# Optimization experiments

Hardware: AMD Instinct MI355X
Metric: run time of the kernel (lower is better)

Reference implementation:

```python
import jax, jax.numpy as jnp
import numpy as np

N_NODES = 50000
N_EDGES = 800000
IN_CH = 64
HEADS = 8
OUT_CH = 8
LEAKY_ALPHA = 0.3  # Keras LeakyReLU default


def setup_inputs() -> dict:
    key = jax.random.key(0)
    k1, k2, k3, k4, k5 = jax.random.split(key, 5)
    h = jax.random.normal(k1, (N_NODES, IN_CH), dtype=jnp.float32)
    W = jax.random.normal(k2, (2 * IN_CH, HEADS * OUT_CH), dtype=jnp.float32) * 0.1
    a = jax.random.normal(k3, (1, HEADS * OUT_CH), dtype=jnp.float32) * 0.1
    src = jax.random.randint(k4, (N_EDGES,), 0, N_NODES, dtype=jnp.int32)
    tgt = jax.random.randint(k5, (N_EDGES,), 0, N_NODES, dtype=jnp.int32)
    return {"h": h, "W": W, "a": a, "src": src, "tgt": tgt}


def reference(h, W, a, src, tgt):
    # h: [N, C]; W: [2C, H*D]; a: [1, H*D]; src/tgt: [E]
    N = h.shape[0]
    hi = h[src]                                   # [E, C] gather source feats
    hj = h[tgt]                                   # [E, C] gather target feats
    hij = jnp.concatenate([hi, hj], axis=-1)      # [E, 2C]
    e = jax.nn.leaky_relu(hij @ W, negative_slope=LEAKY_ALPHA)  # [E, H*D]
    # (dropout omitted: eval mode)
    e = e * a                                     # broadcast attention vector
    e = e.reshape(-1, HEADS, OUT_CH).sum(axis=-1)  # [E, H] per-head logits
    # segment softmax over target nodes (numerically stable)
    m = jax.ops.segment_max(e, tgt, num_segments=N)   # [N, H]
    ex = jnp.exp(e - m[tgt])                          # [E, H]
    s = jax.ops.segment_sum(ex, tgt, num_segments=N)  # [N, H]
    att = ex / s[tgt]                                 # [E, H]
    # weight source features per head (in_channel == head*out_channel branch)
    msg = hi.reshape(-1, HEADS, OUT_CH) * att[:, :, None]  # [E, H, D]
    out = jax.ops.segment_sum(msg.reshape(-1, HEADS * OUT_CH), tgt, num_segments=N)
    return out  # [N, H*D]
```

## Files before the change

kernel.cpp:

```cpp
#include <hip/hip_runtime.h>
#include <hip/hip_fp16.h>
#include <math.h>

#define ALPHA 0.3f
#define MAXDEG 64
#define LOG2E 1.44269504088896f
#define UVOFF (64 * 68 + 4)

__device__ __forceinline__ unsigned int pack2(float u, float hv) {
    __half2 p = __floats2half2_rn(u, hv);
    unsigned int w;
    __builtin_memcpy(&w, &p, 4);
    return w;
}

__device__ __forceinline__ float2 unpack2(unsigned int w) {
    __half2 p;
    __builtin_memcpy(&p, &w, 4);
    return __half22float2(p);
}

__device__ __forceinline__ float dpp_sum8(float z) {
    int t;
    t = __builtin_amdgcn_mov_dpp(__float_as_int(z), 0xB1, 0xF, 0xF, true);
    z += __int_as_float(t);
    t = __builtin_amdgcn_mov_dpp(__float_as_int(z), 0x4E, 0xF, 0xF, true);
    z += __int_as_float(t);
    t = __builtin_amdgcn_mov_dpp(__float_as_int(z), 0x141, 0xF, 0xF, true);
    z += __int_as_float(t);
    return z;
}

__global__ __launch_bounds__(256) void k_prep(const float* __restrict__ h,
                                              const float* __restrict__ W,
                                              const int* __restrict__ src,
                                              const int* __restrict__ tgt,
                                              unsigned int* __restrict__ g,
                                              float* __restrict__ vbuf,
                                              int* __restrict__ cursor,
                                              unsigned short* __restrict__ srcs,
                                              int N, int E, int nUV) {
    __shared__ float Ws[128 * 68 + 4];
    __shared__ float hs[64 * 68];

    if ((int)blockIdx.x >= nUV) {
        const int q = (blockIdx.x - nUV) * 256 + threadIdx.x;
        const int e = q * 4;
        if (e + 4 <= E) {
            const int4 s4 = *(const int4*)(src + e);
            const int4 t4 = *(const int4*)(tgt + e);
            int p;
            p = atomicAdd(&cursor[t4.x], 1); if (p < MAXDEG) srcs[(size_t)t4.x * MAXDEG + p] = (unsigned short)s4.x;
            p = atomicAdd(&cursor[t4.y], 1); if (p < MAXDEG) srcs[(size_t)t4.y * MAXDEG + p] = (unsigned short)s4.y;
            p = atomicAdd(&cursor[t4.z], 1); if (p < MAXDEG) srcs[(size_t)t4.z * MAXDEG + p] = (unsigned short)s4.z;
            p = atomicAdd(&cursor[t4.w], 1); if (p < MAXDEG) srcs[(size_t)t4.w * MAXDEG + p] = (unsigned short)s4.w;
        } else {
            for (int i = e; i < E; ++i) {
                const int ti = tgt[i];
                const int p = atomicAdd(&cursor[ti], 1);
                if (p < MAXDEG) srcs[(size_t)ti * MAXDEG + p] = (unsigned short)src[i];
            }
        }
        return;
    }

    const int t  = threadIdx.x;
    const int nb = blockIdx.x * 64;

    for (int i = t; i < 128 * 64; i += 256) {
        const int row = i >> 6, col = i & 63;
        const int idx = (row < 64) ? (row * 68 + col) : (UVOFF + (row - 64) * 68 + col);
        Ws[idx] = W[i];
    }
    for (int i = t; i < 64 * 64; i += 256) {
        const int nn = i >> 6, c = i & 63;
        const int n = nb + nn;
        hs[nn * 68 + c] = (n < N) ? h[(size_t)n * 64 + c] : 0.0f;
    }
    __syncthreads();

    const int kk = t & 15;
    const int gn = t >> 4;
    const int colbase = (kk * 8) & 63;
    const int wbase   = (kk < 8) ? 0 : UVOFF;

    float acc[4][8];
#pragma unroll
    for (int i = 0; i < 4; ++i)
#pragma unroll
        for (int j = 0; j < 8; ++j) acc[i][j] = 0.0f;

    for (int c4 = 0; c4 < 64; c4 += 4) {
        float hh4[4][4];
#pragma unroll
        for (int i = 0; i < 4; ++i) {
            const float4 tv = *(const float4*)&hs[(gn * 4 + i) * 68 + c4];
            hh4[i][0] = tv.x; hh4[i][1] = tv.y; hh4[i][2] = tv.z; hh4[i][3] = tv.w;
        }
#pragma unroll
        for (int cc = 0; cc < 4; ++cc) {
            const float* wrow = &Ws[wbase + (c4 + cc) * 68 + colbase];
            const float4 w0 = *(const float4*)(wrow);
            const float4 w1 = *(const float4*)(wrow + 4);
            const float wv[8] = {w0.x, w0.y, w0.z, w0.w, w1.x, w1.y, w1.z, w1.w};
#pragma unroll
            for (int i = 0; i < 4; ++i)
#pragma unroll
                for (int j = 0; j < 8; ++j) acc[i][j] += hh4[i][cc] * wv[j];
        }
    }

#pragma unroll
    for (int i = 0; i < 4; ++i) {
        const int n = nb + gn * 4 + i;
        if (n >= N) continue;
        if (kk < 8) {
            unsigned int w[8];
#pragma unroll
            for (int j = 0; j < 8; ++j)
                w[j] = pack2(acc[i][j], hs[(gn * 4 + i) * 68 + colbase + j]);
            uint4 w0 = {w[0], w[1], w[2], w[3]};
            uint4 w1 = {w[4], w[5], w[6], w[7]};
            *(uint4*)&g[(size_t)n * 64 + colbase]     = w0;
            *(uint4*)&g[(size_t)n * 64 + colbase + 4] = w1;
        } else {
            float4 o0 = {acc[i][0], acc[i][1], acc[i][2], acc[i][3]};
            float4 o1 = {acc[i][4], acc[i][5], acc[i][6], acc[i][7]};
            *(float4*)&vbuf[(size_t)n * 64 + colbase]     = o0;
            *(float4*)&vbuf[(size_t)n * 64 + colbase + 4] = o1;
        }
    }
}

__global__ __launch_bounds__(256) void k_node(const unsigned int* __restrict__ g,
                                              const float* __restrict__ vbuf,
                                              const float* __restrict__ a,
                                              const int* __restrict__ cnt,
                                              const unsigned short* __restrict__ srcs,
                                              float* __restrict__ out, int N) {
    const int wid  = (blockIdx.x * 256 + threadIdx.x) >> 6;
    const int lane = threadIdx.x & 63;
    if (wid >= N) return;

    const float v_l = vbuf[(size_t)wid * 64 + lane];
    const float a_l = a[lane] * LOG2E;
    const int num = min(cnt[wid], MAXDEG);
    const int beg = wid * MAXDEG;

    float l_run = 0.0f, acc = 0.0f;

    int k = 0;
    for (; k + 8 <= num; k += 8) {
        const ushort4 sa = *(const ushort4*)(srcs + beg + k);
        const ushort4 sb = *(const ushort4*)(srcs + beg + k + 4);
        unsigned int w[8];
        w[0] = g[(size_t)sa.x * 64 + lane];
        w[1] = g[(size_t)sa.y * 64 + lane];
        w[2] = g[(size_t)sa.z * 64 + lane];
        w[3] = g[(size_t)sa.w * 64 + lane];
        w[4] = g[(size_t)sb.x * 64 + lane];
        w[5] = g[(size_t)sb.y * 64 + lane];
        w[6] = g[(size_t)sb.z * 64 + lane];
        w[7] = g[(size_t)sb.w * 64 + lane];
#pragma unroll
        for (int j = 0; j < 8; ++j) {
            const float2 f = unpack2(w[j]);
            const float q = f.x + v_l;
            float z = fmaxf(q, q * ALPHA) * a_l;
            z = dpp_sum8(z);
            const float p = __builtin_amdgcn_exp2f(z);
            l_run += p;
            acc = fmaf(f.y, p, acc);
        }
    }
    for (; k < num; ++k) {
        const int s = srcs[beg + k];
        const float2 f = unpack2(g[(size_t)s * 64 + lane]);
        const float q = f.x + v_l;
        float z = fmaxf(q, q * ALPHA) * a_l;
        z = dpp_sum8(z);
        const float p = __builtin_amdgcn_exp2f(z);
        l_run += p;
        acc = fmaf(f.y, p, acc);
    }

    out[(size_t)wid * 64 + lane] = (num > 0) ? (acc / l_run) : 0.0f;
}

extern "C" void kernel_launch(void* const* d_in, const int* in_sizes, int n_in,
                              void* d_out, int out_size, void* d_ws, size_t ws_size,
                              hipStream_t stream) {
    const float* h   = (const float*)d_in[0];
    const float* W   = (const float*)d_in[1];
    const float* a   = (const float*)d_in[2];
    const int*   src = (const int*)d_in[3];
    const int*   tgt = (const int*)d_in[4];
    float* out = (float*)d_out;

    const int N = in_sizes[0] / 64;
    const int E = in_sizes[3];

    unsigned int*   g      = (unsigned int*)d_ws;
    float*          vbuf   = (float*)(g + (size_t)N * 64);
    int*            cursor = (int*)(vbuf + (size_t)N * 64);
    unsigned short* srcs   = (unsigned short*)(cursor + N);

    hipMemsetAsync(cursor, 0, (size_t)N * sizeof(int), stream);

    const int nUV   = (N + 63) / 64;
    const int nFILL = (E / 4 + 255) / 256;
    k_prep<<<nUV + nFILL, 256, 0, stream>>>(h, W, src, tgt, g, vbuf, cursor, srcs, N, E, nUV);
    k_node<<<((size_t)N * 64 + 255) / 256, 256, 0, stream>>>(g, vbuf, a, cursor, srcs, out, N);
}
```

Baseline: 108.0 us.

## Split prep kernel, fold cursor zeroing into UV kernel, read h directly

Replaces the memset plus combined prep kernel with three launches: a UV projection kernel that also zeroes the cursor array, a separate fill kernel, and the node kernel. The UV kernel drops the shared-memory staging of h and reads h rows straight from global memory, which shrinks LDS use and may raise occupancy. This removes the memset call but adds a kernel launch, and the fill phase can no longer overlap with the projection blocks. The cursor zeroing is correct only because each block zeroes 256 entries while (N+63)/64 blocks cover N.

```diff
diff --git a/kernel.cpp b/kernel.cpp
--- a/kernel.cpp
+++ b/kernel.cpp
@@ -31,59 +31,36 @@
     return z;
 }
 
-__global__ __launch_bounds__(256) void k_prep(const float* __restrict__ h,
-                                              const float* __restrict__ W,
-                                              const int* __restrict__ src,
-                                              const int* __restrict__ tgt,
-                                              unsigned int* __restrict__ g,
-                                              float* __restrict__ vbuf,
-                                              int* __restrict__ cursor,
-                                              unsigned short* __restrict__ srcs,
-                                              int N, int E, int nUV) {
-    __shared__ float Ws[128 * 68 + 4];
-    __shared__ float hs[64 * 68];
-
-    if ((int)blockIdx.x >= nUV) {
-        const int q = (blockIdx.x - nUV) * 256 + threadIdx.x;
-        const int e = q * 4;
-        if (e + 4 <= E) {
-            const int4 s4 = *(const int4*)(src + e);
-            const int4 t4 = *(const int4*)(tgt + e);
-            int p;
-            p = atomicAdd(&cursor[t4.x], 1); if (p < MAXDEG) srcs[(size_t)t4.x * MAXDEG + p] = (unsigned short)s4.x;
-            p = atomicAdd(&cursor[t4.y], 1); if (p < MAXDEG) srcs[(size_t)t4.y * MAXDEG + p] = (unsigned short)s4.y;
-            p = atomicAdd(&cursor[t4.z], 1); if (p < MAXDEG) srcs[(size_t)t4.z * MAXDEG + p] = (unsigned short)s4.z;
-            p = atomicAdd(&cursor[t4.w], 1); if (p < MAXDEG) srcs[(size_t)t4.w * MAXDEG + p] = (unsigned short)s4.w;
-        } else {
-            for (int i = e; i < E; ++i) {
-                const int ti = tgt[i];
-                const int p = atomicAdd(&cursor[ti], 1);
-                if (p < MAXDEG) srcs[(size_t)ti * MAXDEG + p] = (unsigned short)src[i];
-            }
-        }
-        return;
-    }
-
-    const int t  = threadIdx.x;
-    const int nb = blockIdx.x * 64;
+__global__ __launch_bounds__(256) void k_uv(const float* __restrict__ h,
+                                            const float* __restrict__ W,
+                                            unsigned int* __restrict__ g,
+                                            float* __restrict__ vbuf,
+                                            int* __restrict__ cursor, int N) {
+    __shared__ float Ws[UVOFF + 64 * 68];
+    const int t = threadIdx.x;
+    const int gidx = blockIdx.x * 256 + t;
+    if (gidx < N) cursor[gidx] = 0;
 
     for (int i = t; i < 128 * 64; i += 256) {
         const int row = i >> 6, col = i & 63;
         const int idx = (row < 64) ? (row * 68 + col) : (UVOFF + (row - 64) * 68 + col);
         Ws[idx] = W[i];
     }
-    for (int i = t; i < 64 * 64; i += 256) {
-        const int nn = i >> 6, c = i & 63;
-        const int n = nb + nn;
-        hs[nn * 68 + c] = (n < N) ? h[(size_t)n * 64 + c] : 0.0f;
-    }
     __syncthreads();
 
+    const int nb = blockIdx.x * 64;
     const int kk = t & 15;
     const int gn = t >> 4;
     const int colbase = (kk * 8) & 63;
     const int wbase   = (kk < 8) ? 0 : UVOFF;
 
+    int nidx[4];
+#pragma unroll
+    for (int i = 0; i < 4; ++i) {
+        int n = nb + gn * 4 + i;
+        nidx[i] = (n < N) ? n : (N - 1);
+    }
+
     float acc[4][8];
 #pragma unroll
     for (int i = 0; i < 4; ++i)
@@ -91,11 +68,11 @@
         for (int j = 0; j < 8; ++j) acc[i][j] = 0.0f;
 
     for (int c4 = 0; c4 < 64; c4 += 4) {
-        float hh4[4][4];
+        float hh[4][4];
 #pragma unroll
         for (int i = 0; i < 4; ++i) {
-            const float4 tv = *(const float4*)&hs[(gn * 4 + i) * 68 + c4];
-            hh4[i][0] = tv.x; hh4[i][1] = tv.y; hh4[i][2] = tv.z; hh4[i][3] = tv.w;
+            const float4 tv = *(const float4*)&h[(size_t)nidx[i] * 64 + c4];
+            hh[i][0] = tv.x; hh[i][1] = tv.y; hh[i][2] = tv.z; hh[i][3] = tv.w;
         }
 #pragma unroll
         for (int cc = 0; cc < 4; ++cc) {
@@ -106,7 +83,7 @@
 #pragma unroll
             for (int i = 0; i < 4; ++i)
 #pragma unroll
-                for (int j = 0; j < 8; ++j) acc[i][j] += hh4[i][cc] * wv[j];
+                for (int j = 0; j < 8; ++j) acc[i][j] += hh[i][cc] * wv[j];
         }
     }
 
@@ -115,10 +92,12 @@
         const int n = nb + gn * 4 + i;
         if (n >= N) continue;
         if (kk < 8) {
+            const float4 h0 = *(const float4*)&h[(size_t)n * 64 + colbase];
+            const float4 h1 = *(const float4*)&h[(size_t)n * 64 + colbase + 4];
+            const float hv[8] = {h0.x, h0.y, h0.z, h0.w, h1.x, h1.y, h1.z, h1.w};
             unsigned int w[8];
 #pragma unroll
-            for (int j = 0; j < 8; ++j)
-                w[j] = pack2(acc[i][j], hs[(gn * 4 + i) * 68 + colbase + j]);
+            for (int j = 0; j < 8; ++j) w[j] = pack2(acc[i][j], hv[j]);
             uint4 w0 = {w[0], w[1], w[2], w[3]};
             uint4 w1 = {w[4], w[5], w[6], w[7]};
             *(uint4*)&g[(size_t)n * 64 + colbase]     = w0;
@@ -128,6 +107,29 @@
             float4 o1 = {acc[i][4], acc[i][5], acc[i][6], acc[i][7]};
             *(float4*)&vbuf[(size_t)n * 64 + colbase]     = o0;
             *(float4*)&vbuf[(size_t)n * 64 + colbase + 4] = o1;
+        }
+    }
+}
+
+__global__ __launch_bounds__(256) void k_fill(const int* __restrict__ src,
+                                              const int* __restrict__ tgt,
+                                              int* __restrict__ cursor,
+                                              unsigned short* __restrict__ srcs, int E) {
+    const int q = blockIdx.x * 256 + threadIdx.x;
+    const int e = q * 4;
+    if (e + 4 <= E) {
+        const int4 s4 = *(const int4*)(src + e);
+        const int4 t4 = *(const int4*)(tgt + e);
+        int p;
+        p = atomicAdd(&cursor[t4.x], 1); if (p < MAXDEG) srcs[(size_t)t4.x * MAXDEG + p] = (unsigned short)s4.x;
+        p = atomicAdd(&cursor[t4.y], 1); if (p < MAXDEG) srcs[(size_t)t4.y * MAXDEG + p] = (unsigned short)s4.y;
+        p = atomicAdd(&cursor[t4.z], 1); if (p < MAXDEG) srcs[(size_t)t4.z * MAXDEG + p] = (unsigned short)s4.z;
+        p = atomicAdd(&cursor[t4.w], 1); if (p < MAXDEG) srcs[(size_t)t4.w * MAXDEG + p] = (unsigned short)s4.w;
+    } else {
+        for (int i = e; i < E; ++i) {
+            const int ti = tgt[i];
+            const int p = atomicAdd(&cursor[ti], 1);
+            if (p < MAXDEG) srcs[(size_t)ti * MAXDEG + p] = (unsigned short)src[i];
         }
     }
 }
@@ -205,10 +207,7 @@
     int*            cursor = (int*)(vbuf + (size_t)N * 64);
     unsigned short* srcs   = (unsigned short*)(cursor + N);
 
-    hipMemsetAsync(cursor, 0, (size_t)N * sizeof(int), stream);
-
-    const int nUV   = (N + 63) / 64;
-    const int nFILL = (E / 4 + 255) / 256;
-    k_prep<<<nUV + nFILL, 256, 0, stream>>>(h, W, src, tgt, g, vbuf, cursor, srcs, N, E, nUV);
+    k_uv<<<(N + 63) / 64, 256, 0, stream>>>(h, W, g, vbuf, cursor, N);
+    k_fill<<<(E / 4 + 255) / 256, 256, 0, stream>>>(src, tgt, cursor, srcs, E);
     k_node<<<((size_t)N * 64 + 255) / 256, 256, 0, stream>>>(g, vbuf, a, cursor, srcs, out, N);
 }
```

Result: no change. 106.6 us (-1.3%).
